# Kernel optimization log

Measured on AMD Instinct MI355X. Metric: run time of the kernel, lower is better.

Reference implementation:

```python
import jax, jax.numpy as jnp
import numpy as np

B, S = 65536, 128          # batch of tasks, support set size
MAX_CLASSES = 10
STATS_DIM = MAX_CLASSES + 4  # hist + [n_nonzero, entropy, subset_size, hist_max]
TOKEN_DIM = 256


def setup_inputs() -> dict:
    key = jax.random.key(0)
    k1, k2, k3, k4, k5 = jax.random.split(key, 5)
    y_support = jax.random.randint(k1, (B, S), 0, MAX_CLASSES, dtype=jnp.int32)
    # MLP params: Linear(14, D) -> GELU -> Linear(D, D)
    w1 = jax.random.normal(k2, (STATS_DIM, TOKEN_DIM), jnp.float32) / np.sqrt(STATS_DIM)
    b1 = jax.random.normal(k3, (TOKEN_DIM,), jnp.float32) * 0.01
    w2 = jax.random.normal(k4, (TOKEN_DIM, TOKEN_DIM), jnp.float32) / np.sqrt(TOKEN_DIM)
    b2 = jax.random.normal(k5, (TOKEN_DIM,), jnp.float32) * 0.01
    return {"y_support": y_support, "w1": w1, "b1": b1, "w2": w2, "b2": b2}


def reference(y_support, w1, b1, w2, b2):
    b, s = y_support.shape
    # Batched bincount via scatter-add: hist[i, c] = #{j : y_support[i, j] == c}
    rows = jnp.arange(b, dtype=jnp.int32)[:, None]              # [B, 1]
    hist = jnp.zeros((b, MAX_CLASSES), jnp.float32).at[rows, y_support].add(1.0)
    total = jnp.maximum(hist.sum(axis=-1, keepdims=True), 1.0)  # clamp_min(1.0)
    p = hist / total                                            # [B, C]
    entropy = -(p * jnp.log(p + 1e-6)).sum(axis=-1)             # [B]
    n_nonzero = (p > 0).sum(axis=-1).astype(jnp.float32)        # [B]
    stats = jnp.concatenate([
        p,
        n_nonzero[:, None],
        entropy[:, None],
        jnp.full((b, 1), float(s), jnp.float32),
        p.max(axis=-1, keepdims=True),
    ], axis=1)                                                  # [B, C+4]
    h = jax.nn.gelu(stats @ w1 + b1, approximate=False)         # exact GELU like nn.GELU
    return h @ w2 + b2                                          # [B, TOKEN_DIM]
```

## Files before the change

### kernel.cpp

```cpp
#include <hip/hip_runtime.h>
#include <hip/hip_bf16.h>
#include <stdint.h>


#define SSUP 128
#define DD   256

typedef __attribute__((ext_vector_type(8)))  short bf16x8;
typedef __attribute__((ext_vector_type(16))) float f32x16;

__device__ __forceinline__ unsigned f2bf_u(float f) {
    union { float f; unsigned u; } v; v.f = f;
    return (v.u + 0x7FFFu + ((v.u >> 16) & 1u)) >> 16;
}
__device__ __forceinline__ unsigned pk2(float a, float b) {
    return f2bf_u(a) | (f2bf_u(b) << 16);
}
__device__ __forceinline__ unsigned pk2f(float a, float b) {
    union { __hip_bfloat162 h; unsigned u; } cv;
    cv.h = __float22bfloat162_rn(make_float2(a, b));
    return cv.u;
}

__device__ __forceinline__ float gelu_f(float x) {
    float t = x * x;
    float u = __builtin_fmaf(t, -0.0713548162726f, -1.5957691216057f);
    float e = __expf(x * u);
    return x * __builtin_amdgcn_rcpf(1.0f + e);
}

__global__ void prep_kernel(const float* __restrict__ w1,
                            const float* __restrict__ w2,
                            unsigned short* __restrict__ w1f,
                            unsigned short* __restrict__ w2f) {
    int tid = blockIdx.x * 256 + threadIdx.x;
    if (tid < 8192) {
        int l  = tid & 63;
        int nt = (tid >> 6) & 7;
        int s  = tid >> 9;
        int n  = nt * 32 + (l & 31);
        int k0 = s * 16 + (l >> 5) * 8;
        unsigned pk[4];
        #pragma unroll
        for (int h = 0; h < 4; ++h)
            pk[h] = pk2(w2[(size_t)(k0 + 2*h) * DD + n],
                        w2[(size_t)(k0 + 2*h + 1) * DD + n]);
        *(uint4*)&w2f[(size_t)tid * 8] = make_uint4(pk[0], pk[1], pk[2], pk[3]);
    } else if (tid < 8704) {
        int idx = tid - 8192;
        int l   = idx & 63;
        int nt  = idx >> 6;
        int n   = nt * 32 + (l & 31);
        int kk0 = (l >> 5) * 8;
        unsigned pk[4];
        #pragma unroll
        for (int h = 0; h < 4; ++h) {
            int ka = kk0 + 2*h, kb = kk0 + 2*h + 1;
            float fa = (ka < 14) ? w1[(size_t)ka * DD + n] : 0.0f;
            float fb = (kb < 14) ? w1[(size_t)kb * DD + n] : 0.0f;
            pk[h] = pk2(fa, fb);
        }
        *(uint4*)&w1f[(size_t)idx * 8] = make_uint4(pk[0], pk[1], pk[2], pk[3]);
    }
}

__global__ __launch_bounds__(256, 8)
void encoder_kernel(const int* __restrict__ y,
                    const float* __restrict__ b1,
                    const float* __restrict__ b2,
                    const unsigned short* __restrict__ w1f,
                    const unsigned short* __restrict__ w2f,
                    float* __restrict__ out) {
    __shared__ __align__(16) unsigned stats_lds[64][4];
    __shared__ __align__(16) float stage[16 * 260];
    unsigned short* hb = (unsigned short*)stage;

    const int tid  = threadIdx.x;
    const int lane = tid & 63;
    const int wid  = tid >> 6;
    const int l31  = lane & 31;
    const int lh   = lane >> 5;
    const int rbase = blockIdx.x * 32;

    const int hrow = wid * 8 + (lane >> 3);
    const int sub  = lane & 7;
    const int4* yp = (const int4*)(y + (size_t)(rbase + hrow) * SSUP);
    unsigned long long pk = 0ull;
    #pragma unroll
    for (int i = 0; i < 4; ++i) {
        int4 v = yp[i * 8 + sub];
        pk += 1ull << (6 * v.x);
        pk += 1ull << (6 * v.y);
        pk += 1ull << (6 * v.z);
        pk += 1ull << (6 * v.w);
    }
    pk += __shfl_xor((long long)pk, 1);
    float p[10]; float ent = 0.f, pmax = 0.f, nnz = 0.f;
    #pragma unroll
    for (int c = 0; c < 10; ++c) {
        int cc = (int)((pk >> (6 * c)) & 63ull);
        cc += __shfl_xor(cc, 2);
        cc += __shfl_xor(cc, 4);
        float pc = (float)cc * 0.0078125f;
        p[c] = pc;
        nnz += (cc > 0) ? 1.0f : 0.0f;
        ent -= pc * __logf(pc + 1e-6f);
        pmax = fmaxf(pmax, pc);
    }
    if (sub < 2) {
        uint4 st;
        if (sub == 0) st = make_uint4(pk2f(p[0], p[1]), pk2f(p[2], p[3]),
                                      pk2f(p[4], p[5]), pk2f(p[6], p[7]));
        else          st = make_uint4(pk2f(p[8], p[9]), pk2f(nnz, ent),
                                      pk2f(128.0f, pmax), 0u);
        *(uint4*)&stats_lds[hrow * 2 + sub][0] = st;
    }
    __syncthreads();

    union { unsigned u[4]; bf16x8 v; } sf;
    *(uint4*)sf.u = *(const uint4*)&stats_lds[l31 * 2 + lh][0];
    const bf16x8 sfrag = sf.v;

    #pragma unroll
    for (int t = 0; t < 2; ++t) {
        const int nt = wid * 2 + t;
        union { unsigned u[4]; bf16x8 v; } wf;
        *(uint4*)wf.u = *(const uint4*)&w1f[(size_t)(nt * 64 + lane) * 8];
        f32x16 c;
        #pragma unroll
        for (int g = 0; g < 4; ++g) {
            float4 bv = *(const float4*)&b1[nt * 32 + 8 * g + 4 * lh];
            c[4*g+0] = bv.x; c[4*g+1] = bv.y; c[4*g+2] = bv.z; c[4*g+3] = bv.w;
        }
        c = __builtin_amdgcn_mfma_f32_32x32x16_bf16(wf.v, sfrag, c, 0, 0, 0);
        unsigned own[8], rcv[8];
        #pragma unroll
        for (int g = 0; g < 4; ++g) {
            own[2*g+0] = pk2f(gelu_f(c[4*g+0]), gelu_f(c[4*g+1]));
            own[2*g+1] = pk2f(gelu_f(c[4*g+2]), gelu_f(c[4*g+3]));
        }
        #pragma unroll
        for (int j = 0; j < 8; ++j) rcv[j] = (unsigned)__shfl_xor((int)own[j], 32);
        #pragma unroll
        for (int tt = 0; tt < 2; ++tt) {
            const int s = 2 * nt + tt;
            uint4 fr;
            fr.x = lh ? rcv[4*tt+2] : own[4*tt+0];
            fr.y = lh ? rcv[4*tt+3] : own[4*tt+1];
            fr.z = lh ? own[4*tt+2] : rcv[4*tt+0];
            fr.w = lh ? own[4*tt+3] : rcv[4*tt+1];
            *(uint4*)&hb[(size_t)((s * 2 + lh) * 32 + l31) * 8] = fr;
        }
    }
    __syncthreads();

    f32x16 acc[2];
    #pragma unroll
    for (int u = 0; u < 2; ++u) {
        const int nt = wid * 2 + u;
        #pragma unroll
        for (int g = 0; g < 4; ++g) {
            float4 bv = *(const float4*)&b2[nt * 32 + 8 * g + 4 * lh];
            acc[u][4*g+0] = bv.x; acc[u][4*g+1] = bv.y;
            acc[u][4*g+2] = bv.z; acc[u][4*g+3] = bv.w;
        }
    }
    #pragma unroll
    for (int s = 0; s < 16; ++s) {
        union { unsigned u[4]; bf16x8 v; } hf;
        *(uint4*)hf.u = *(const uint4*)&hb[(size_t)((s * 2 + lh) * 32 + l31) * 8];
        #pragma unroll
        for (int u = 0; u < 2; ++u) {
            const int nt = wid * 2 + u;
            union { unsigned u[4]; bf16x8 v; } wf;
            *(uint4*)wf.u = *(const uint4*)&w2f[(size_t)((s * 8 + nt) * 64 + lane) * 8];
            acc[u] = __builtin_amdgcn_mfma_f32_32x32x16_bf16(wf.v, hf.v, acc[u], 0, 0, 0);
        }
    }

    #pragma unroll
    for (int h = 0; h < 2; ++h) {
        __syncthreads();
        if ((l31 >> 4) == h) {
            const int r = l31 & 15;
            #pragma unroll
            for (int u = 0; u < 2; ++u) {
                const int nt = wid * 2 + u;
                #pragma unroll
                for (int g = 0; g < 4; ++g) {
                    float4 o;
                    o.x = acc[u][4*g+0]; o.y = acc[u][4*g+1];
                    o.z = acc[u][4*g+2]; o.w = acc[u][4*g+3];
                    *(float4*)&stage[r * 260 + nt * 32 + 8 * g + 4 * lh] = o;
                }
            }
        }
        __syncthreads();
        #pragma unroll
        for (int g2 = 0; g2 < 4; ++g2) {
            const int rl = wid * 4 + g2;
            float4 v = *(const float4*)&stage[rl * 260 + lane * 4];
            *(float4*)&out[(size_t)(rbase + h * 16 + rl) * DD + lane * 4] = v;
        }
    }
}

extern "C" void kernel_launch(void* const* d_in, const int* in_sizes, int n_in,
                              void* d_out, int out_size, void* d_ws, size_t ws_size,
                              hipStream_t stream) {
    const int*   y  = (const int*)d_in[0];
    const float* w1 = (const float*)d_in[1];
    const float* b1 = (const float*)d_in[2];
    const float* w2 = (const float*)d_in[3];
    const float* b2 = (const float*)d_in[4];
    float* out = (float*)d_out;

    unsigned short* w2f = (unsigned short*)d_ws;
    unsigned short* w1f = w2f + 65536;

    prep_kernel<<<34, 256, 0, stream>>>(w1, w2, w1f, w2f);

    const int nrows = in_sizes[0] / SSUP;
    encoder_kernel<<<nrows / 32, 256, 0, stream>>>(y, b1, b2, w1f, w2f, out);
}
```

Baseline: 108.0 us.

## Process 64 rows per block to reuse each W2 fragment across two row groups

Each block now handles 64 rows instead of 32, split into two 32-row groups. Every W2 fragment loaded from global or L2 feeds two MFMAs instead of one, which halves weight-load traffic per output row. In exchange the block uses twice the LDS staging and more accumulator registers, launch bounds drop to 4 blocks per SM, and there are half as many blocks.

After: 107.7 us. About the same (-0.3%).

```diff
diff --git a/kernel.cpp b/kernel.cpp
--- a/kernel.cpp
+++ b/kernel.cpp
@@ -64,143 +64,161 @@
     }
 }
 
-__global__ __launch_bounds__(256, 8)
+__global__ __launch_bounds__(256, 4)
 void encoder_kernel(const int* __restrict__ y,
                     const float* __restrict__ b1,
                     const float* __restrict__ b2,
                     const unsigned short* __restrict__ w1f,
                     const unsigned short* __restrict__ w2f,
                     float* __restrict__ out) {
-    __shared__ __align__(16) unsigned stats_lds[64][4];
-    __shared__ __align__(16) float stage[16 * 260];
-    unsigned short* hb = (unsigned short*)stage;
+    __shared__ __align__(16) unsigned stats_lds[128][4];
+    __shared__ __align__(16) float stage[32 * 260];
+    unsigned short* hb0 = (unsigned short*)stage;
+    unsigned short* hb1 = hb0 + 16 * 2 * 32 * 8;
 
     const int tid  = threadIdx.x;
     const int lane = tid & 63;
     const int wid  = tid >> 6;
     const int l31  = lane & 31;
     const int lh   = lane >> 5;
-    const int rbase = blockIdx.x * 32;
-
-    const int hrow = wid * 8 + (lane >> 3);
-    const int sub  = lane & 7;
-    const int4* yp = (const int4*)(y + (size_t)(rbase + hrow) * SSUP);
-    unsigned long long pk = 0ull;
-    #pragma unroll
-    for (int i = 0; i < 4; ++i) {
-        int4 v = yp[i * 8 + sub];
-        pk += 1ull << (6 * v.x);
-        pk += 1ull << (6 * v.y);
-        pk += 1ull << (6 * v.z);
-        pk += 1ull << (6 * v.w);
-    }
-    pk += __shfl_xor((long long)pk, 1);
-    float p[10]; float ent = 0.f, pmax = 0.f, nnz = 0.f;
-    #pragma unroll
-    for (int c = 0; c < 10; ++c) {
-        int cc = (int)((pk >> (6 * c)) & 63ull);
-        cc += __shfl_xor(cc, 2);
-        cc += __shfl_xor(cc, 4);
-        float pc = (float)cc * 0.0078125f;
-        p[c] = pc;
-        nnz += (cc > 0) ? 1.0f : 0.0f;
-        ent -= pc * __logf(pc + 1e-6f);
-        pmax = fmaxf(pmax, pc);
-    }
-    if (sub < 2) {
-        uint4 st;
-        if (sub == 0) st = make_uint4(pk2f(p[0], p[1]), pk2f(p[2], p[3]),
-                                      pk2f(p[4], p[5]), pk2f(p[6], p[7]));
-        else          st = make_uint4(pk2f(p[8], p[9]), pk2f(nnz, ent),
-                                      pk2f(128.0f, pmax), 0u);
-        *(uint4*)&stats_lds[hrow * 2 + sub][0] = st;
+    const int rbase = blockIdx.x * 64;
+
+    const int sub = lane & 7;
+    #pragma unroll
+    for (int rr = 0; rr < 2; ++rr) {
+        const int hrow = wid * 16 + rr * 8 + (lane >> 3);
+        const int4* yp = (const int4*)(y + (size_t)(rbase + hrow) * SSUP);
+        unsigned long long pk = 0ull;
+        #pragma unroll
+        for (int i = 0; i < 4; ++i) {
+            int4 v = yp[i * 8 + sub];
+            pk += 1ull << (6 * v.x);
+            pk += 1ull << (6 * v.y);
+            pk += 1ull << (6 * v.z);
+            pk += 1ull << (6 * v.w);
+        }
+        pk += __shfl_xor((long long)pk, 1);
+        float p[10]; float ent = 0.f, pmax = 0.f, nnz = 0.f;
+        #pragma unroll
+        for (int c = 0; c < 10; ++c) {
+            int cc = (int)((pk >> (6 * c)) & 63ull);
+            cc += __shfl_xor(cc, 2);
+            cc += __shfl_xor(cc, 4);
+            float pc = (float)cc * 0.0078125f;
+            p[c] = pc;
+            nnz += (cc > 0) ? 1.0f : 0.0f;
+            ent -= pc * __logf(pc + 1e-6f);
+            pmax = fmaxf(pmax, pc);
+        }
+        if (sub < 2) {
+            uint4 st;
+            if (sub == 0) st = make_uint4(pk2f(p[0], p[1]), pk2f(p[2], p[3]),
+                                          pk2f(p[4], p[5]), pk2f(p[6], p[7]));
+            else          st = make_uint4(pk2f(p[8], p[9]), pk2f(nnz, ent),
+                                          pk2f(128.0f, pmax), 0u);
+            *(uint4*)&stats_lds[hrow * 2 + sub][0] = st;
+        }
     }
     __syncthreads();
 
-    union { unsigned u[4]; bf16x8 v; } sf;
-    *(uint4*)sf.u = *(const uint4*)&stats_lds[l31 * 2 + lh][0];
-    const bf16x8 sfrag = sf.v;
+    bf16x8 sfrag[2];
+    #pragma unroll
+    for (int rg = 0; rg < 2; ++rg) {
+        union { unsigned u[4]; bf16x8 v; } sf;
+        *(uint4*)sf.u = *(const uint4*)&stats_lds[(rg * 32 + l31) * 2 + lh][0];
+        sfrag[rg] = sf.v;
+    }
 
     #pragma unroll
     for (int t = 0; t < 2; ++t) {
         const int nt = wid * 2 + t;
         union { unsigned u[4]; bf16x8 v; } wf;
         *(uint4*)wf.u = *(const uint4*)&w1f[(size_t)(nt * 64 + lane) * 8];
-        f32x16 c;
-        #pragma unroll
-        for (int g = 0; g < 4; ++g) {
-            float4 bv = *(const float4*)&b1[nt * 32 + 8 * g + 4 * lh];
-            c[4*g+0] = bv.x; c[4*g+1] = bv.y; c[4*g+2] = bv.z; c[4*g+3] = bv.w;
-        }
-        c = __builtin_amdgcn_mfma_f32_32x32x16_bf16(wf.v, sfrag, c, 0, 0, 0);
-        unsigned own[8], rcv[8];
-        #pragma unroll
-        for (int g = 0; g < 4; ++g) {
-            own[2*g+0] = pk2f(gelu_f(c[4*g+0]), gelu_f(c[4*g+1]));
-            own[2*g+1] = pk2f(gelu_f(c[4*g+2]), gelu_f(c[4*g+3]));
-        }
-        #pragma unroll
-        for (int j = 0; j < 8; ++j) rcv[j] = (unsigned)__shfl_xor((int)own[j], 32);
-        #pragma unroll
-        for (int tt = 0; tt < 2; ++tt) {
-            const int s = 2 * nt + tt;
-            uint4 fr;
-            fr.x = lh ? rcv[4*tt+2] : own[4*tt+0];
-            fr.y = lh ? rcv[4*tt+3] : own[4*tt+1];
-            fr.z = lh ? own[4*tt+2] : rcv[4*tt+0];
-            fr.w = lh ? own[4*tt+3] : rcv[4*tt+1];
-            *(uint4*)&hb[(size_t)((s * 2 + lh) * 32 + l31) * 8] = fr;
+        #pragma unroll
+        for (int rg = 0; rg < 2; ++rg) {
+            unsigned short* hb = rg ? hb1 : hb0;
+            f32x16 c;
+            #pragma unroll
+            for (int g = 0; g < 4; ++g) {
+                float4 bv = *(const float4*)&b1[nt * 32 + 8 * g + 4 * lh];
+                c[4*g+0] = bv.x; c[4*g+1] = bv.y;
+                c[4*g+2] = bv.z; c[4*g+3] = bv.w;
+            }
+            c = __builtin_amdgcn_mfma_f32_32x32x16_bf16(wf.v, sfrag[rg], c, 0, 0, 0);
+            unsigned own[8], rcv[8];
+            #pragma unroll
+            for (int g = 0; g < 4; ++g) {
+                own[2*g+0] = pk2f(gelu_f(c[4*g+0]), gelu_f(c[4*g+1]));
+                own[2*g+1] = pk2f(gelu_f(c[4*g+2]), gelu_f(c[4*g+3]));
+            }
+            #pragma unroll
+            for (int j = 0; j < 8; ++j) rcv[j] = (unsigned)__shfl_xor((int)own[j], 32);
+            #pragma unroll
+            for (int tt = 0; tt < 2; ++tt) {
+                const int s = 2 * nt + tt;
+                uint4 fr;
+                fr.x = lh ? rcv[4*tt+2] : own[4*tt+0];
+                fr.y = lh ? rcv[4*tt+3] : own[4*tt+1];
+                fr.z = lh ? own[4*tt+2] : rcv[4*tt+0];
+                fr.w = lh ? own[4*tt+3] : rcv[4*tt+1];
+                *(uint4*)&hb[(size_t)((s * 2 + lh) * 32 + l31) * 8] = fr;
+            }
         }
     }
     __syncthreads();
 
-    f32x16 acc[2];
+    f32x16 acc[2][2];
     #pragma unroll
     for (int u = 0; u < 2; ++u) {
         const int nt = wid * 2 + u;
         #pragma unroll
         for (int g = 0; g < 4; ++g) {
             float4 bv = *(const float4*)&b2[nt * 32 + 8 * g + 4 * lh];
-            acc[u][4*g+0] = bv.x; acc[u][4*g+1] = bv.y;
-            acc[u][4*g+2] = bv.z; acc[u][4*g+3] = bv.w;
+            #pragma unroll
+            for (int rg = 0; rg < 2; ++rg) {
+                acc[rg][u][4*g+0] = bv.x; acc[rg][u][4*g+1] = bv.y;
+                acc[rg][u][4*g+2] = bv.z; acc[rg][u][4*g+3] = bv.w;
+            }
         }
     }
     #pragma unroll
     for (int s = 0; s < 16; ++s) {
-        union { unsigned u[4]; bf16x8 v; } hf;
-        *(uint4*)hf.u = *(const uint4*)&hb[(size_t)((s * 2 + lh) * 32 + l31) * 8];
+        union { unsigned u[4]; bf16x8 v; } hf[2], wf[2];
+        *(uint4*)hf[0].u = *(const uint4*)&hb0[(size_t)((s * 2 + lh) * 32 + l31) * 8];
+        *(uint4*)hf[1].u = *(const uint4*)&hb1[(size_t)((s * 2 + lh) * 32 + l31) * 8];
         #pragma unroll
         for (int u = 0; u < 2; ++u) {
             const int nt = wid * 2 + u;
-            union { unsigned u[4]; bf16x8 v; } wf;
-            *(uint4*)wf.u = *(const uint4*)&w2f[(size_t)((s * 8 + nt) * 64 + lane) * 8];
-            acc[u] = __builtin_amdgcn_mfma_f32_32x32x16_bf16(wf.v, hf.v, acc[u], 0, 0, 0);
-        }
-    }
-
-    #pragma unroll
-    for (int h = 0; h < 2; ++h) {
+            *(uint4*)wf[u].u = *(const uint4*)&w2f[(size_t)((s * 8 + nt) * 64 + lane) * 8];
+        }
+        #pragma unroll
+        for (int rg = 0; rg < 2; ++rg)
+            #pragma unroll
+            for (int u = 0; u < 2; ++u)
+                acc[rg][u] = __builtin_amdgcn_mfma_f32_32x32x16_bf16(
+                    wf[u].v, hf[rg].v, acc[rg][u], 0, 0, 0);
+    }
+
+    #pragma unroll
+    for (int rg = 0; rg < 2; ++rg) {
         __syncthreads();
-        if ((l31 >> 4) == h) {
-            const int r = l31 & 15;
-            #pragma unroll
-            for (int u = 0; u < 2; ++u) {
-                const int nt = wid * 2 + u;
-                #pragma unroll
-                for (int g = 0; g < 4; ++g) {
-                    float4 o;
-                    o.x = acc[u][4*g+0]; o.y = acc[u][4*g+1];
-                    o.z = acc[u][4*g+2]; o.w = acc[u][4*g+3];
-                    *(float4*)&stage[r * 260 + nt * 32 + 8 * g + 4 * lh] = o;
-                }
+        #pragma unroll
+        for (int u = 0; u < 2; ++u) {
+            const int nt = wid * 2 + u;
+            #pragma unroll
+            for (int g = 0; g < 4; ++g) {
+                float4 o;
+                o.x = acc[rg][u][4*g+0]; o.y = acc[rg][u][4*g+1];
+                o.z = acc[rg][u][4*g+2]; o.w = acc[rg][u][4*g+3];
+                *(float4*)&stage[l31 * 260 + nt * 32 + 8 * g + 4 * lh] = o;
             }
         }
         __syncthreads();
         #pragma unroll
-        for (int g2 = 0; g2 < 4; ++g2) {
-            const int rl = wid * 4 + g2;
+        for (int g2 = 0; g2 < 8; ++g2) {
+            const int rl = wid * 8 + g2;
             float4 v = *(const float4*)&stage[rl * 260 + lane * 4];
-            *(float4*)&out[(size_t)(rbase + h * 16 + rl) * DD + lane * 4] = v;
+            *(float4*)&out[(size_t)(rbase + rg * 32 + rl) * DD + lane * 4] = v;
         }
     }
 }
@@ -221,5 +239,5 @@
     prep_kernel<<<34, 256, 0, stream>>>(w1, w2, w1f, w2f);
 
     const int nrows = in_sizes[0] / SSUP;
-    encoder_kernel<<<nrows / 32, 256, 0, stream>>>(y, b1, b2, w1f, w2f, out);
-}
+    encoder_kernel<<<nrows / 64, 256, 0, stream>>>(y, b1, b2, w1f, w2f, out);
+}
```
